# Optimization experiments

Hardware: AMD Instinct MI355X
Metric: run time of the kernel (lower is better)

The kernel has to match this reference:

```python
import jax, jax.numpy as jnp
import numpy as np

FEATURE_DIM = 512
HIDDEN_DIM = 512
N_HEADS = 8
HEAD_DIM = HIDDEN_DIM // N_HEADS
MAX_LEN = 5000
GAMMA = 0.5  # gaussian relative-position bias width
LN_EPS = 1e-5


def make_pe(d_model, max_len):
    # sinusoidal positional encoding buffer, as in PositionalEncoding.__init__
    pos = jnp.arange(max_len, dtype=jnp.float32)[:, None]
    div = jnp.exp(jnp.arange(0, d_model, 2, dtype=jnp.float32) * (-np.log(10000.0) / d_model))
    ang = pos * div  # [max_len, d_model/2]
    pe = jnp.zeros((max_len, d_model), dtype=jnp.float32)
    pe = pe.at[:, 0::2].set(jnp.sin(ang)).at[:, 1::2].set(jnp.cos(ang))
    return pe


def setup_inputs() -> dict:
    key = jax.random.key(0)
    k_x, k_q, k_k, k_v = jax.random.split(key, 4)
    xavier = np.sqrt(6.0 / (FEATURE_DIM + HEAD_DIM))  # xavier_uniform over last two dims
    return {
        "data_window": jax.random.normal(k_x, (1, 2048, FEATURE_DIM), dtype=jnp.float32),
        "W_query": jax.random.uniform(k_q, (N_HEADS, FEATURE_DIM, HEAD_DIM), jnp.float32, -xavier, xavier),
        "W_key": jax.random.uniform(k_k, (N_HEADS, FEATURE_DIM, HEAD_DIM), jnp.float32, -xavier, xavier),
        "W_value": jax.random.uniform(k_v, (N_HEADS, FEATURE_DIM, HEAD_DIM), jnp.float32, -xavier, xavier),
        "ln_gamma": jnp.ones((FEATURE_DIM,), dtype=jnp.float32),
        "ln_beta": jnp.zeros((FEATURE_DIM,), dtype=jnp.float32),
    }


def reference(data_window, W_query, W_key, W_value, ln_gamma, ln_beta):
    B, S, F = data_window.shape
    temperature = 1.0

    # LayerNorm over feature dim
    mu = jnp.mean(data_window, axis=-1, keepdims=True)
    var = jnp.mean(jnp.square(data_window - mu), axis=-1, keepdims=True)
    x = (data_window - mu) * jax.lax.rsqrt(var + LN_EPS) * ln_gamma + ln_beta

    # positional encoding, exactly as original: x + pe[:x.shape[0]] (requires B==1)
    pe = make_pe(FEATURE_DIM, MAX_LEN)
    x = x + pe[:B]  # [B,F] broadcasts over [B,S,F] only because B==1

    # per-head QKV projections, vectorized over heads
    Q = jnp.einsum('bsf,hfd->bhsd', x, W_query)
    K = jnp.einsum('bsf,hfd->bhsd', x, W_key)
    V = jnp.einsum('bsf,hfd->bhsd', x, W_value)

    scores = jnp.einsum('bhsd,bhtd->bhst', Q, K) / np.sqrt(HEAD_DIM)

    # gaussian relative-position bias: scale(=1) * exp(-gamma * (i-j)^2)
    p = jnp.arange(S, dtype=jnp.float32)
    rel = p[:, None] - p[None, :]
    bias = jnp.exp(-GAMMA * jnp.square(rel))  # [S,S]
    scores = (scores + bias[None, None]) / temperature
    # dropout on scores is identity in eval mode

    attn = jax.nn.softmax(scores, axis=-1)  # [B,H,S,S]
    head_out = jnp.einsum('bhst,bhtd->bhsd', attn, V)

    # concat heads along feature dim: [B,S,H*D]
    multi_head_output = head_out.transpose(0, 2, 1, 3).reshape(B, S, N_HEADS * HEAD_DIM)
    mean_weights = jnp.mean(attn, axis=1)  # [B,S,S]
    return multi_head_output, mean_weights
```

## Files before the change

### kernel.cpp

```cpp
#include <hip/hip_runtime.h>
#include <hip/hip_bf16.h>
#include <math.h>

#define S_LEN 2048
#define FDIM  512
#define NH    8
#define HD    64
#define MH_ELEMS (S_LEN * FDIM)
#define MEAN_ELEMS (S_LEN * S_LEN)

typedef _Float16 half_t;
typedef _Float16 half2v __attribute__((ext_vector_type(2)));
typedef _Float16 half4v __attribute__((ext_vector_type(4)));
typedef _Float16 half8v __attribute__((ext_vector_type(8)));
typedef float    float4v __attribute__((ext_vector_type(4)));
typedef int      int4v   __attribute__((ext_vector_type(4)));
typedef unsigned short ushort4v __attribute__((ext_vector_type(4)));

#define MFMA16(a, b, c) __builtin_amdgcn_mfma_f32_16x16x32_f16((a), (b), (c), 0, 0, 0)

static __device__ __forceinline__ unsigned short f2bf(float x) {
    union { __hip_bfloat16 b; unsigned short u; } cv;
    cv.b = __float2bfloat16(x);
    return cv.u;
}

__global__ __launch_bounds__(256) void ln_pe_kernel(const float* __restrict__ x,
                                                    const float* __restrict__ gamma,
                                                    const float* __restrict__ beta,
                                                    half_t* __restrict__ xo) {
    const int row = blockIdx.x;
    const int tid = threadIdx.x;
    const float2 v = ((const float2*)(x + (size_t)row * FDIM))[tid];
    float s = v.x + v.y;
    float q = v.x * v.x + v.y * v.y;
    #pragma unroll
    for (int off = 1; off < 64; off <<= 1) {
        s += __shfl_xor(s, off, 64);
        q += __shfl_xor(q, off, 64);
    }
    __shared__ float red[8];
    const int wave = tid >> 6;
    if ((tid & 63) == 0) { red[wave] = s; red[4 + wave] = q; }
    __syncthreads();
    s = red[0] + red[1] + red[2] + red[3];
    q = red[4] + red[5] + red[6] + red[7];
    const float mu  = s * (1.0f / FDIM);
    const float var = q * (1.0f / FDIM) - mu * mu;
    const float rstd = rsqrtf(var + 1e-5f);
    const int f0 = tid * 2, f1 = tid * 2 + 1;
    const float o0 = (v.x - mu) * rstd * gamma[f0] + beta[f0];
    const float o1 = (v.y - mu) * rstd * gamma[f1] + beta[f1] + 1.0f;
    half2v o; o.x = (half_t)o0; o.y = (half_t)o1;
    ((half2v*)(xo + (size_t)row * FDIM))[tid] = o;
}

__global__ __launch_bounds__(256) void wt_kernel(const float* __restrict__ Wq,
                                                 const float* __restrict__ Wk,
                                                 const float* __restrict__ Wv,
                                                 half_t* __restrict__ WT) {
    const int k0 = blockIdx.x * 64;
    const int h  = blockIdx.y, z = blockIdx.z;
    const float* W = ((z == 0) ? Wq : (z == 1) ? Wk : Wv) + (size_t)h * FDIM * HD;
    __shared__ float Ls[64][65];
    const int tid = threadIdx.x;
    {
        const int kk = tid >> 2, dg = (tid & 3) * 16;
        #pragma unroll
        for (int j = 0; j < 4; ++j) {
            const float4 w = *(const float4*)(W + (size_t)(k0 + kk) * HD + dg + j * 4);
            Ls[kk][dg + j * 4 + 0] = w.x; Ls[kk][dg + j * 4 + 1] = w.y;
            Ls[kk][dg + j * 4 + 2] = w.z; Ls[kk][dg + j * 4 + 3] = w.w;
        }
    }
    __syncthreads();
    {
        const int d = tid >> 2, kg = (tid & 3) * 16;
        half8v t0, t1;
        #pragma unroll
        for (int j = 0; j < 8; ++j) t0[j] = (half_t)Ls[kg + j][d];
        #pragma unroll
        for (int j = 0; j < 8; ++j) t1[j] = (half_t)Ls[kg + 8 + j][d];
        half_t* dst = WT + ((size_t)(z * NH + h) * HD + d) * FDIM + k0 + kg;
        *(half8v*)dst = t0;
        *(half8v*)(dst + 8) = t1;
    }
}

__global__ __launch_bounds__(256) void qkv_kernel(const half_t* __restrict__ xh,
                                                  const half_t* __restrict__ WT,
                                                  half_t* __restrict__ Qo,
                                                  half_t* __restrict__ Ko,
                                                  half_t* __restrict__ VTo) {
    const int ms0 = blockIdx.x * 64;
    const int h   = blockIdx.y, z = blockIdx.z;
    const half_t* Wt = WT + (size_t)(z * NH + h) * HD * FDIM;

    const int tid = threadIdx.x;
    const int wv = tid >> 6, lane = tid & 63;
    const int lo = lane & 15, qq = lane >> 4;

    float4v acc[4];
    #pragma unroll
    for (int cg = 0; cg < 4; ++cg) acc[cg] = (float4v){0.f, 0.f, 0.f, 0.f};

    const half_t* arow = xh + (size_t)(ms0 + wv * 16 + lo) * FDIM + qq * 8;
    const half_t* wrow[4];
    #pragma unroll
    for (int cg = 0; cg < 4; ++cg) wrow[cg] = Wt + (size_t)(cg * 16 + lo) * FDIM + qq * 8;

    half8v a0 = *(const half8v*)(arow), a1 = *(const half8v*)(arow + 32);
    half8v b0[4], b1[4];
    #pragma unroll
    for (int cg = 0; cg < 4; ++cg) { b0[cg] = *(const half8v*)(wrow[cg]); b1[cg] = *(const half8v*)(wrow[cg] + 32); }

    for (int k0 = 0; k0 < FDIM; k0 += 64) {
        const int kn0 = (k0 + 64 < FDIM) ? k0 + 64 : 0;
        const int kn1 = (k0 + 96 < FDIM) ? k0 + 96 : 0;
        half8v an0 = *(const half8v*)(arow + kn0);
        half8v bn0[4];
        #pragma unroll
        for (int cg = 0; cg < 4; ++cg) bn0[cg] = *(const half8v*)(wrow[cg] + kn0);
        #pragma unroll
        for (int cg = 0; cg < 4; ++cg) acc[cg] = MFMA16(a0, b0[cg], acc[cg]);
        half8v an1 = *(const half8v*)(arow + kn1);
        half8v bn1[4];
        #pragma unroll
        for (int cg = 0; cg < 4; ++cg) bn1[cg] = *(const half8v*)(wrow[cg] + kn1);
        #pragma unroll
        for (int cg = 0; cg < 4; ++cg) acc[cg] = MFMA16(a1, b1[cg], acc[cg]);
        a0 = an0; a1 = an1;
        #pragma unroll
        for (int cg = 0; cg < 4; ++cg) { b0[cg] = bn0[cg]; b1[cg] = bn1[cg]; }
    }

    __shared__ float Ls[64][65];
    if (z < 2) {
        half_t* Co = ((z == 0) ? Qo : Ko) + (size_t)h * S_LEN * HD;
        #pragma unroll
        for (int cg = 0; cg < 4; ++cg)
            #pragma unroll
            for (int r = 0; r < 4; ++r)
                Co[(size_t)(ms0 + wv * 16 + qq * 4 + r) * HD + cg * 16 + lo] = (half_t)acc[cg][r];
    } else {
        #pragma unroll
        for (int cg = 0; cg < 4; ++cg)
            #pragma unroll
            for (int r = 0; r < 4; ++r)
                Ls[wv * 16 + qq * 4 + r][cg * 16 + lo] = acc[cg][r];
        __syncthreads();
        const int d = tid & 63, sg = tid >> 6;
        half8v t0, t1;
        #pragma unroll
        for (int j = 0; j < 8; ++j) t0[j] = (half_t)Ls[sg * 16 + j][d];
        #pragma unroll
        for (int j = 0; j < 8; ++j) t1[j] = (half_t)Ls[sg * 16 + 8 + j][d];
        half_t* dst = VTo + (size_t)(h * HD + d) * S_LEN + ms0 + sg * 16;
        *(half8v*)dst = t0;
        *(half8v*)(dst + 8) = t1;
    }
}

__global__ __launch_bounds__(256) void attn2_kernel(const half_t* __restrict__ Qw,
                                                    const half_t* __restrict__ Kw,
                                                    const half_t* __restrict__ VT,
                                                    unsigned short* __restrict__ Praw,
                                                    half_t* __restrict__ Op,
                                                    float* __restrict__ mp,
                                                    float* __restrict__ lp) {
    const int s0 = blockIdx.x * 16;
    const int h  = blockIdx.y;
    const int z  = blockIdx.z;
    const half_t* Qh = Qw + (size_t)h * S_LEN * HD;
    const half_t* Kh = Kw + (size_t)h * S_LEN * HD;
    const half_t* Vt = VT + (size_t)h * (size_t)HD * S_LEN;

    __shared__ float Osh[4][16][65];
    __shared__ float lsh[4][16];
    __shared__ float msh[4][16];

    const int tid = threadIdx.x;
    const int wv = tid >> 6, lane = tid & 63;
    const int lo = lane & 15, qq = lane >> 4;
    const int tb = z * 1024 + wv * 256;

    const half8v q0 = *(const half8v*)(Qh + (size_t)(s0 + lo) * HD + qq * 8);
    const half8v q1 = *(const half8v*)(Qh + (size_t)(s0 + lo) * HD + 32 + qq * 8);

    float4v accO[4];
    #pragma unroll
    for (int dt = 0; dt < 4; ++dt) accO[dt] = (float4v){0.f, 0.f, 0.f, 0.f};
    float m = 0.f;
    float lsum = 0.f;

    const int srcLow  = lo + ((qq & 1) * 2) * 16;
    const int srcHigh = srcLow + 16;
    const bool sel1 = (qq >> 1) != 0;

    unsigned short* prb = Praw + ((size_t)h << 22) + (size_t)(s0 + lo) * S_LEN + qq * 4;

    half8v kc[4], vc[4];
    {
        const half_t* kp0 = Kh + (size_t)(tb + lo) * HD;
        const half_t* kp1 = Kh + (size_t)(tb + 16 + lo) * HD;
        kc[0] = *(const half8v*)(kp0 + qq * 8);
        kc[1] = *(const half8v*)(kp0 + 32 + qq * 8);
        kc[2] = *(const half8v*)(kp1 + qq * 8);
        kc[3] = *(const half8v*)(kp1 + 32 + qq * 8);
        #pragma unroll
        for (int dt = 0; dt < 4; ++dt)
            vc[dt] = *(const half8v*)(Vt + (size_t)(dt * 16 + lo) * S_LEN + tb + qq * 8);
    }

    for (int ps = 0; ps < 8; ++ps) {
        const int Tg  = tb + ps * 32;
        const int Tgn = tb + ((ps < 7) ? ps + 1 : ps) * 32;
        half8v kn[4], vn[4];
        {
            const half_t* kp0 = Kh + (size_t)(Tgn + lo) * HD;
            const half_t* kp1 = Kh + (size_t)(Tgn + 16 + lo) * HD;
            kn[0] = *(const half8v*)(kp0 + qq * 8);
            kn[1] = *(const half8v*)(kp0 + 32 + qq * 8);
            kn[2] = *(const half8v*)(kp1 + qq * 8);
            kn[3] = *(const half8v*)(kp1 + 32 + qq * 8);
            #pragma unroll
            for (int dt = 0; dt < 4; ++dt)
                vn[dt] = *(const half8v*)(Vt + (size_t)(dt * 16 + lo) * S_LEN + Tgn + qq * 8);
        }
        float4v c0 = (float4v){0.f, 0.f, 0.f, 0.f};
        c0 = MFMA16(kc[0], q0, c0);
        c0 = MFMA16(kc[1], q1, c0);
        float4v c1 = (float4v){0.f, 0.f, 0.f, 0.f};
        c1 = MFMA16(kc[2], q0, c1);
        c1 = MFMA16(kc[3], q1, c1);

        float S0[4], S1[4];
        const int dd0 = s0 - Tg;
        const bool near0 = (dd0 > -40) && (dd0 < 40);
        const bool near1 = (dd0 - 16 > -40) && (dd0 - 16 < 40);
        #pragma unroll
        for (int r = 0; r < 4; ++r) {
            float s = c0[r] * 0.125f;
            if (near0) {
                const float d = (float)(s0 + lo - (Tg + qq * 4 + r));
                s += __expf(-0.5f * d * d);
            }
            S0[r] = s;
            float t = c1[r] * 0.125f;
            if (near1) {
                const float d = (float)(s0 + lo - (Tg + 16 + qq * 4 + r));
                t += __expf(-0.5f * d * d);
            }
            S1[r] = t;
        }
        float smax = fmaxf(fmaxf(fmaxf(S0[0], S0[1]), fmaxf(S0[2], S0[3])),
                           fmaxf(fmaxf(S1[0], S1[1]), fmaxf(S1[2], S1[3])));
        smax = fmaxf(smax, __shfl_xor(smax, 16, 64));
        smax = fmaxf(smax, __shfl_xor(smax, 32, 64));
        const float mn = fmaxf(m, smax);
        const float alpha = __expf(m - mn);
        m = mn;
        float E0[4], E1[4];
        float ls = 0.f;
        #pragma unroll
        for (int r = 0; r < 4; ++r) {
            E0[r] = __expf(S0[r] - mn);
            E1[r] = __expf(S1[r] - mn);
            ls += E0[r] + E1[r];
        }
        lsum = lsum * alpha + ls;
        #pragma unroll
        for (int dt = 0; dt < 4; ++dt)
            #pragma unroll
            for (int i = 0; i < 4; ++i) accO[dt][i] *= alpha;

        {
            const float emn = __expf(mn);
            ushort4v ep0, ep1;
            #pragma unroll
            for (int r = 0; r < 4; ++r) {
                ep0[r] = f2bf(E0[r] * emn);
                ep1[r] = f2bf(E1[r] * emn);
            }
            unsigned short* pr = prb + Tg;
            *(ushort4v*)pr = ep0;
            *(ushort4v*)(pr + 16) = ep1;
        }

        int pk0, pk1, pk2, pk3;
        {
            half2v p;
            p.x = (half_t)E0[0]; p.y = (half_t)E0[1];
            pk0 = __builtin_bit_cast(int, p);
            p.x = (half_t)E0[2]; p.y = (half_t)E0[3];
            pk1 = __builtin_bit_cast(int, p);
            p.x = (half_t)E1[0]; p.y = (half_t)E1[1];
            pk2 = __builtin_bit_cast(int, p);
            p.x = (half_t)E1[2]; p.y = (half_t)E1[3];
            pk3 = __builtin_bit_cast(int, p);
        }
        int4v bi;
        {
            const int l0a = __shfl(pk0, srcLow, 64),  l0b = __shfl(pk2, srcLow, 64);
            const int l1a = __shfl(pk1, srcLow, 64),  l1b = __shfl(pk3, srcLow, 64);
            const int h0a = __shfl(pk0, srcHigh, 64), h0b = __shfl(pk2, srcHigh, 64);
            const int h1a = __shfl(pk1, srcHigh, 64), h1b = __shfl(pk3, srcHigh, 64);
            bi[0] = sel1 ? l0b : l0a;
            bi[1] = sel1 ? l1b : l1a;
            bi[2] = sel1 ? h0b : h0a;
            bi[3] = sel1 ? h1b : h1a;
        }
        const half8v bp = __builtin_bit_cast(half8v, bi);
        #pragma unroll
        for (int dt = 0; dt < 4; ++dt) accO[dt] = MFMA16(vc[dt], bp, accO[dt]);

        #pragma unroll
        for (int i = 0; i < 4; ++i) { kc[i] = kn[i]; vc[i] = vn[i]; }
    }

    lsum += __shfl_xor(lsum, 16, 64);
    lsum += __shfl_xor(lsum, 32, 64);
    if (qq == 0) { lsh[wv][lo] = lsum; msh[wv][lo] = m; }
    #pragma unroll
    for (int dt = 0; dt < 4; ++dt)
        #pragma unroll
        for (int r = 0; r < 4; ++r)
            Osh[wv][lo][dt * 16 + qq * 4 + r] = accO[dt][r];
    __syncthreads();

    {
        const int q = tid >> 4, dg = tid & 15;
        const float m0 = msh[0][q], m1 = msh[1][q], m2 = msh[2][q], m3 = msh[3][q];
        const float M = fmaxf(fmaxf(m0, m1), fmaxf(m2, m3));
        const float f0 = __expf(m0 - M), f1 = __expf(m1 - M);
        const float f2 = __expf(m2 - M), f3 = __expf(m3 - M);
        const float L = lsh[0][q] * f0 + lsh[1][q] * f1 + lsh[2][q] * f2 + lsh[3][q] * f3;
        half4v o;
        #pragma unroll
        for (int i = 0; i < 4; ++i) {
            const float ov = Osh[0][q][dg * 4 + i] * f0 + Osh[1][q][dg * 4 + i] * f1 +
                             Osh[2][q][dg * 4 + i] * f2 + Osh[3][q][dg * 4 + i] * f3;
            o[i] = (half_t)ov;
        }
        const size_t pidx = (size_t)(z * NH + h) * S_LEN + s0 + q;
        *(half4v*)(Op + pidx * HD + dg * 4) = o;
        if (dg == 0) { mp[pidx] = M; lp[pidx] = L; }
    }
}

__global__ __launch_bounds__(256) void merge_kernel(const half_t* __restrict__ Op,
                                                    const float* __restrict__ mp,
                                                    const float* __restrict__ lp,
                                                    float* __restrict__ linv,
                                                    float* __restrict__ out) {
    const int s0 = blockIdx.x * 16, h = blockIdx.y;
    const int tid = threadIdx.x, q = tid >> 4, dg = tid & 15;
    const size_t i0 = (size_t)h * S_LEN + s0 + q;
    const size_t i1 = (size_t)(NH + h) * S_LEN + s0 + q;
    const float m0 = mp[i0], m1 = mp[i1], l0 = lp[i0], l1 = lp[i1];
    const float M = fmaxf(m0, m1);
    const float f0 = __expf(m0 - M), f1 = __expf(m1 - M);
    const float L = l0 * f0 + l1 * f1;
    const float inv = 1.0f / L;
    const half4v o0 = *(const half4v*)(Op + i0 * HD + dg * 4);
    const half4v o1 = *(const half4v*)(Op + i1 * HD + dg * 4);
    float4 o;
    o.x = ((float)o0[0] * f0 + (float)o1[0] * f1) * inv;
    o.y = ((float)o0[1] * f0 + (float)o1[1] * f1) * inv;
    o.z = ((float)o0[2] * f0 + (float)o1[2] * f1) * inv;
    o.w = ((float)o0[3] * f0 + (float)o1[3] * f1) * inv;
    *(float4*)(out + (size_t)(s0 + q) * FDIM + h * HD + dg * 4) = o;
    if (dg == 0) linv[(size_t)h * S_LEN + s0 + q] = __expf(-M) * inv;
}

__global__ __launch_bounds__(256) void mean_kernel(const unsigned short* __restrict__ Praw,
                                                   const float* __restrict__ linv,
                                                   float* __restrict__ out) {
    const size_t idx = ((size_t)blockIdx.x * 256 + threadIdx.x) * 8;
    const int q = (int)(idx >> 11);
    float acc[8] = {0.f, 0.f, 0.f, 0.f, 0.f, 0.f, 0.f, 0.f};
    #pragma unroll
    for (int h = 0; h < NH; ++h) {
        const uint4 u = *(const uint4*)(Praw + ((size_t)h << 22) + idx);
        const float li = linv[h * S_LEN + q];
        const unsigned int uu[4] = {u.x, u.y, u.z, u.w};
        #pragma unroll
        for (int j = 0; j < 4; ++j) {
            const float a = __builtin_bit_cast(float, uu[j] << 16);
            const float b = __builtin_bit_cast(float, uu[j] & 0xFFFF0000u);
            acc[2 * j]     += a * li;
            acc[2 * j + 1] += b * li;
        }
    }
    float* o = out + MH_ELEMS + idx;
    *(float4*)o       = make_float4(acc[0] * 0.125f, acc[1] * 0.125f, acc[2] * 0.125f, acc[3] * 0.125f);
    *(float4*)(o + 4) = make_float4(acc[4] * 0.125f, acc[5] * 0.125f, acc[6] * 0.125f, acc[7] * 0.125f);
}

extern "C" void kernel_launch(void* const* d_in, const int* in_sizes, int n_in,
                              void* d_out, int out_size, void* d_ws, size_t ws_size,
                              hipStream_t stream) {
    const float* x  = (const float*)d_in[0];
    const float* Wq = (const float*)d_in[1];
    const float* Wk = (const float*)d_in[2];
    const float* Wv = (const float*)d_in[3];
    const float* g  = (const float*)d_in[4];
    const float* b  = (const float*)d_in[5];
    float* out = (float*)d_out;
    char*  ws  = (char*)d_ws;

    half_t* Qh   = (half_t*)(ws);
    half_t* Kh   = (half_t*)(ws + (2ull  << 20));
    half_t* VT   = (half_t*)(ws + (4ull  << 20));
    half_t* xh   = (half_t*)(ws + (6ull  << 20));
    half_t* WT   = (half_t*)(ws + (8ull  << 20));
    half_t* Op   = (half_t*)(ws + (10ull << 20));
    float*  mp   = (float*) (ws + (14ull << 20));
    float*  lp   = (float*) (ws + (14ull << 20) + (128ull << 10));
    float*  linv = (float*) (ws + (14ull << 20) + (512ull << 10));
    unsigned short* Praw = (unsigned short*)(ws + (16ull << 20));

    ln_pe_kernel<<<S_LEN, 256, 0, stream>>>(x, g, b, xh);
    wt_kernel<<<dim3(8, 8, 3), 256, 0, stream>>>(Wq, Wk, Wv, WT);
    qkv_kernel<<<dim3(32, 8, 3), 256, 0, stream>>>(xh, WT, Qh, Kh, VT);
    attn2_kernel<<<dim3(128, 8, 2), 256, 0, stream>>>(Qh, Kh, VT, Praw, Op, mp, lp);
    merge_kernel<<<dim3(128, 8), 256, 0, stream>>>(Op, mp, lp, linv, out);
    mean_kernel<<<MEAN_ELEMS / 8 / 256, 256, 0, stream>>>(Praw, linv, out);
}
```

Measured before the change: 185.1 us.

## Fuse prep and merge kernels, double per-block rows in QKV and attention

```diff
diff --git a/kernel.cpp b/kernel.cpp
--- a/kernel.cpp
+++ b/kernel.cpp
@@ -25,65 +25,67 @@
     return cv.u;
 }
 
-__global__ __launch_bounds__(256) void ln_pe_kernel(const float* __restrict__ x,
-                                                    const float* __restrict__ gamma,
-                                                    const float* __restrict__ beta,
-                                                    half_t* __restrict__ xo) {
-    const int row = blockIdx.x;
+__global__ __launch_bounds__(256) void prep_kernel(const float* __restrict__ x,
+                                                   const float* __restrict__ gamma,
+                                                   const float* __restrict__ beta,
+                                                   const float* __restrict__ Wq,
+                                                   const float* __restrict__ Wk,
+                                                   const float* __restrict__ Wv,
+                                                   half_t* __restrict__ xo,
+                                                   half_t* __restrict__ WT) {
     const int tid = threadIdx.x;
-    const float2 v = ((const float2*)(x + (size_t)row * FDIM))[tid];
-    float s = v.x + v.y;
-    float q = v.x * v.x + v.y * v.y;
-    #pragma unroll
-    for (int off = 1; off < 64; off <<= 1) {
-        s += __shfl_xor(s, off, 64);
-        q += __shfl_xor(q, off, 64);
-    }
-    __shared__ float red[8];
-    const int wave = tid >> 6;
-    if ((tid & 63) == 0) { red[wave] = s; red[4 + wave] = q; }
-    __syncthreads();
-    s = red[0] + red[1] + red[2] + red[3];
-    q = red[4] + red[5] + red[6] + red[7];
-    const float mu  = s * (1.0f / FDIM);
-    const float var = q * (1.0f / FDIM) - mu * mu;
-    const float rstd = rsqrtf(var + 1e-5f);
-    const int f0 = tid * 2, f1 = tid * 2 + 1;
-    const float o0 = (v.x - mu) * rstd * gamma[f0] + beta[f0];
-    const float o1 = (v.y - mu) * rstd * gamma[f1] + beta[f1] + 1.0f;
-    half2v o; o.x = (half_t)o0; o.y = (half_t)o1;
-    ((half2v*)(xo + (size_t)row * FDIM))[tid] = o;
-}
-
-__global__ __launch_bounds__(256) void wt_kernel(const float* __restrict__ Wq,
-                                                 const float* __restrict__ Wk,
-                                                 const float* __restrict__ Wv,
-                                                 half_t* __restrict__ WT) {
-    const int k0 = blockIdx.x * 64;
-    const int h  = blockIdx.y, z = blockIdx.z;
-    const float* W = ((z == 0) ? Wq : (z == 1) ? Wk : Wv) + (size_t)h * FDIM * HD;
-    __shared__ float Ls[64][65];
-    const int tid = threadIdx.x;
-    {
-        const int kk = tid >> 2, dg = (tid & 3) * 16;
-        #pragma unroll
-        for (int j = 0; j < 4; ++j) {
-            const float4 w = *(const float4*)(W + (size_t)(k0 + kk) * HD + dg + j * 4);
-            Ls[kk][dg + j * 4 + 0] = w.x; Ls[kk][dg + j * 4 + 1] = w.y;
-            Ls[kk][dg + j * 4 + 2] = w.z; Ls[kk][dg + j * 4 + 3] = w.w;
-        }
-    }
-    __syncthreads();
-    {
-        const int d = tid >> 2, kg = (tid & 3) * 16;
-        half8v t0, t1;
-        #pragma unroll
-        for (int j = 0; j < 8; ++j) t0[j] = (half_t)Ls[kg + j][d];
-        #pragma unroll
-        for (int j = 0; j < 8; ++j) t1[j] = (half_t)Ls[kg + 8 + j][d];
-        half_t* dst = WT + ((size_t)(z * NH + h) * HD + d) * FDIM + k0 + kg;
-        *(half8v*)dst = t0;
-        *(half8v*)(dst + 8) = t1;
+    if (blockIdx.x < 2048) {
+        const int row = blockIdx.x;
+        const float2 v = ((const float2*)(x + (size_t)row * FDIM))[tid];
+        float s = v.x + v.y;
+        float q = v.x * v.x + v.y * v.y;
+        #pragma unroll
+        for (int off = 1; off < 64; off <<= 1) {
+            s += __shfl_xor(s, off, 64);
+            q += __shfl_xor(q, off, 64);
+        }
+        __shared__ float red[8];
+        const int wave = tid >> 6;
+        if ((tid & 63) == 0) { red[wave] = s; red[4 + wave] = q; }
+        __syncthreads();
+        s = red[0] + red[1] + red[2] + red[3];
+        q = red[4] + red[5] + red[6] + red[7];
+        const float mu  = s * (1.0f / FDIM);
+        const float var = q * (1.0f / FDIM) - mu * mu;
+        const float rstd = rsqrtf(var + 1e-5f);
+        const int f0 = tid * 2, f1 = tid * 2 + 1;
+        const float o0 = (v.x - mu) * rstd * gamma[f0] + beta[f0];
+        const float o1 = (v.y - mu) * rstd * gamma[f1] + beta[f1] + 1.0f;
+        half2v o; o.x = (half_t)o0; o.y = (half_t)o1;
+        ((half2v*)(xo + (size_t)row * FDIM))[tid] = o;
+    } else {
+        const int idx = blockIdx.x - 2048;
+        const int k0 = (idx & 7) * 64;
+        const int h  = (idx >> 3) & 7;
+        const int z  = idx >> 6;
+        const float* W = ((z == 0) ? Wq : (z == 1) ? Wk : Wv) + (size_t)h * FDIM * HD;
+        __shared__ float Ls[64][65];
+        {
+            const int kk = tid >> 2, dg = (tid & 3) * 16;
+            #pragma unroll
+            for (int j = 0; j < 4; ++j) {
+                const float4 w = *(const float4*)(W + (size_t)(k0 + kk) * HD + dg + j * 4);
+                Ls[kk][dg + j * 4 + 0] = w.x; Ls[kk][dg + j * 4 + 1] = w.y;
+                Ls[kk][dg + j * 4 + 2] = w.z; Ls[kk][dg + j * 4 + 3] = w.w;
+            }
+        }
+        __syncthreads();
+        {
+            const int d = tid >> 2, kg = (tid & 3) * 16;
+            half8v t0, t1;
+            #pragma unroll
+            for (int j = 0; j < 8; ++j) t0[j] = (half_t)Ls[kg + j][d];
+            #pragma unroll
+            for (int j = 0; j < 8; ++j) t1[j] = (half_t)Ls[kg + 8 + j][d];
+            half_t* dst = WT + ((size_t)(z * NH + h) * HD + d) * FDIM + k0 + kg;
+            *(half8v*)dst = t0;
+            *(half8v*)(dst + 8) = t1;
+        }
     }
 }
 
@@ -92,7 +94,7 @@
                                                   half_t* __restrict__ Qo,
                                                   half_t* __restrict__ Ko,
                                                   half_t* __restrict__ VTo) {
-    const int ms0 = blockIdx.x * 64;
+    const int ms0 = blockIdx.x * 128;
     const int h   = blockIdx.y, z = blockIdx.z;
     const half_t* Wt = WT + (size_t)(z * NH + h) * HD * FDIM;
 
@@ -100,64 +102,75 @@
     const int wv = tid >> 6, lane = tid & 63;
     const int lo = lane & 15, qq = lane >> 4;
 
-    float4v acc[4];
-    #pragma unroll
-    for (int cg = 0; cg < 4; ++cg) acc[cg] = (float4v){0.f, 0.f, 0.f, 0.f};
-
-    const half_t* arow = xh + (size_t)(ms0 + wv * 16 + lo) * FDIM + qq * 8;
+    float4v acc[2][4];
+    #pragma unroll
+    for (int rg = 0; rg < 2; ++rg)
+        #pragma unroll
+        for (int cg = 0; cg < 4; ++cg) acc[rg][cg] = (float4v){0.f, 0.f, 0.f, 0.f};
+
+    const half_t* ar[2];
+    ar[0] = xh + (size_t)(ms0 + wv * 32 + lo) * FDIM + qq * 8;
+    ar[1] = ar[0] + 16 * FDIM;
     const half_t* wrow[4];
     #pragma unroll
     for (int cg = 0; cg < 4; ++cg) wrow[cg] = Wt + (size_t)(cg * 16 + lo) * FDIM + qq * 8;
 
-    half8v a0 = *(const half8v*)(arow), a1 = *(const half8v*)(arow + 32);
-    half8v b0[4], b1[4];
-    #pragma unroll
-    for (int cg = 0; cg < 4; ++cg) { b0[cg] = *(const half8v*)(wrow[cg]); b1[cg] = *(const half8v*)(wrow[cg] + 32); }
+    half8v a_c[2][2], b_c[4][2];
+    #pragma unroll
+    for (int rg = 0; rg < 2; ++rg) { a_c[rg][0] = *(const half8v*)(ar[rg]); a_c[rg][1] = *(const half8v*)(ar[rg] + 32); }
+    #pragma unroll
+    for (int cg = 0; cg < 4; ++cg) { b_c[cg][0] = *(const half8v*)(wrow[cg]); b_c[cg][1] = *(const half8v*)(wrow[cg] + 32); }
 
     for (int k0 = 0; k0 < FDIM; k0 += 64) {
         const int kn0 = (k0 + 64 < FDIM) ? k0 + 64 : 0;
         const int kn1 = (k0 + 96 < FDIM) ? k0 + 96 : 0;
-        half8v an0 = *(const half8v*)(arow + kn0);
-        half8v bn0[4];
-        #pragma unroll
-        for (int cg = 0; cg < 4; ++cg) bn0[cg] = *(const half8v*)(wrow[cg] + kn0);
-        #pragma unroll
-        for (int cg = 0; cg < 4; ++cg) acc[cg] = MFMA16(a0, b0[cg], acc[cg]);
-        half8v an1 = *(const half8v*)(arow + kn1);
-        half8v bn1[4];
-        #pragma unroll
-        for (int cg = 0; cg < 4; ++cg) bn1[cg] = *(const half8v*)(wrow[cg] + kn1);
-        #pragma unroll
-        for (int cg = 0; cg < 4; ++cg) acc[cg] = MFMA16(a1, b1[cg], acc[cg]);
-        a0 = an0; a1 = an1;
-        #pragma unroll
-        for (int cg = 0; cg < 4; ++cg) { b0[cg] = bn0[cg]; b1[cg] = bn1[cg]; }
-    }
-
-    __shared__ float Ls[64][65];
+        half8v a_n[2][2], b_n[4][2];
+        #pragma unroll
+        for (int rg = 0; rg < 2; ++rg) { a_n[rg][0] = *(const half8v*)(ar[rg] + kn0); a_n[rg][1] = *(const half8v*)(ar[rg] + kn1); }
+        #pragma unroll
+        for (int cg = 0; cg < 4; ++cg) { b_n[cg][0] = *(const half8v*)(wrow[cg] + kn0); b_n[cg][1] = *(const half8v*)(wrow[cg] + kn1); }
+        #pragma unroll
+        for (int kh = 0; kh < 2; ++kh)
+            #pragma unroll
+            for (int rg = 0; rg < 2; ++rg)
+                #pragma unroll
+                for (int cg = 0; cg < 4; ++cg)
+                    acc[rg][cg] = MFMA16(a_c[rg][kh], b_c[cg][kh], acc[rg][cg]);
+        #pragma unroll
+        for (int rg = 0; rg < 2; ++rg) { a_c[rg][0] = a_n[rg][0]; a_c[rg][1] = a_n[rg][1]; }
+        #pragma unroll
+        for (int cg = 0; cg < 4; ++cg) { b_c[cg][0] = b_n[cg][0]; b_c[cg][1] = b_n[cg][1]; }
+    }
+
     if (z < 2) {
         half_t* Co = ((z == 0) ? Qo : Ko) + (size_t)h * S_LEN * HD;
         #pragma unroll
-        for (int cg = 0; cg < 4; ++cg)
-            #pragma unroll
-            for (int r = 0; r < 4; ++r)
-                Co[(size_t)(ms0 + wv * 16 + qq * 4 + r) * HD + cg * 16 + lo] = (half_t)acc[cg][r];
+        for (int rg = 0; rg < 2; ++rg)
+            #pragma unroll
+            for (int cg = 0; cg < 4; ++cg)
+                #pragma unroll
+                for (int r = 0; r < 4; ++r)
+                    Co[(size_t)(ms0 + wv * 32 + rg * 16 + qq * 4 + r) * HD + cg * 16 + lo] =
+                        (half_t)acc[rg][cg][r];
     } else {
-        #pragma unroll
-        for (int cg = 0; cg < 4; ++cg)
-            #pragma unroll
-            for (int r = 0; r < 4; ++r)
-                Ls[wv * 16 + qq * 4 + r][cg * 16 + lo] = acc[cg][r];
+        __shared__ float Ls[128][65];
+        #pragma unroll
+        for (int rg = 0; rg < 2; ++rg)
+            #pragma unroll
+            for (int cg = 0; cg < 4; ++cg)
+                #pragma unroll
+                for (int r = 0; r < 4; ++r)
+                    Ls[wv * 32 + rg * 16 + qq * 4 + r][cg * 16 + lo] = acc[rg][cg][r];
         __syncthreads();
         const int d = tid & 63, sg = tid >> 6;
-        half8v t0, t1;
-        #pragma unroll
-        for (int j = 0; j < 8; ++j) t0[j] = (half_t)Ls[sg * 16 + j][d];
-        #pragma unroll
-        for (int j = 0; j < 8; ++j) t1[j] = (half_t)Ls[sg * 16 + 8 + j][d];
-        half_t* dst = VTo + (size_t)(h * HD + d) * S_LEN + ms0 + sg * 16;
-        *(half8v*)dst = t0;
-        *(half8v*)(dst + 8) = t1;
+        half_t* dst = VTo + (size_t)(h * HD + d) * S_LEN + ms0 + sg * 32;
+        #pragma unroll
+        for (int c = 0; c < 4; ++c) {
+            half8v t;
+            #pragma unroll
+            for (int j = 0; j < 8; ++j) t[j] = (half_t)Ls[sg * 32 + c * 8 + j][d];
+            *(half8v*)(dst + c * 8) = t;
+        }
     }
 }
 
@@ -168,38 +181,43 @@
                                                     half_t* __restrict__ Op,
                                                     float* __restrict__ mp,
                                                     float* __restrict__ lp) {
-    const int s0 = blockIdx.x * 16;
+    const int s0 = blockIdx.x * 32;
     const int h  = blockIdx.y;
     const int z  = blockIdx.z;
     const half_t* Qh = Qw + (size_t)h * S_LEN * HD;
     const half_t* Kh = Kw + (size_t)h * S_LEN * HD;
     const half_t* Vt = VT + (size_t)h * (size_t)HD * S_LEN;
 
-    __shared__ float Osh[4][16][65];
-    __shared__ float lsh[4][16];
-    __shared__ float msh[4][16];
+    __shared__ float Osh[4][32][65];
+    __shared__ float lsh[4][32];
+    __shared__ float msh[4][32];
 
     const int tid = threadIdx.x;
     const int wv = tid >> 6, lane = tid & 63;
     const int lo = lane & 15, qq = lane >> 4;
     const int tb = z * 1024 + wv * 256;
 
-    const half8v q0 = *(const half8v*)(Qh + (size_t)(s0 + lo) * HD + qq * 8);
-    const half8v q1 = *(const half8v*)(Qh + (size_t)(s0 + lo) * HD + 32 + qq * 8);
-
-    float4v accO[4];
-    #pragma unroll
-    for (int dt = 0; dt < 4; ++dt) accO[dt] = (float4v){0.f, 0.f, 0.f, 0.f};
-    float m = 0.f;
-    float lsum = 0.f;
+    const half8v qA0 = *(const half8v*)(Qh + (size_t)(s0 + lo) * HD + qq * 8);
+    const half8v qA1 = *(const half8v*)(Qh + (size_t)(s0 + lo) * HD + 32 + qq * 8);
+    const half8v qB0 = *(const half8v*)(Qh + (size_t)(s0 + 16 + lo) * HD + qq * 8);
+    const half8v qB1 = *(const half8v*)(Qh + (size_t)(s0 + 16 + lo) * HD + 32 + qq * 8);
+
+    float4v accA[4], accB[4];
+    #pragma unroll
+    for (int dt = 0; dt < 4; ++dt) {
+        accA[dt] = (float4v){0.f, 0.f, 0.f, 0.f};
+        accB[dt] = (float4v){0.f, 0.f, 0.f, 0.f};
+    }
+    float mA = 0.f, mB = 0.f, lA = 0.f, lB = 0.f;
 
     const int srcLow  = lo + ((qq & 1) * 2) * 16;
     const int srcHigh = srcLow + 16;
     const bool sel1 = (qq >> 1) != 0;
 
-    unsigned short* prb = Praw + ((size_t)h << 22) + (size_t)(s0 + lo) * S_LEN + qq * 4;
-
-    half8v kc[4], vc[4];
+    unsigned short* prA = Praw + ((size_t)h << 22) + (size_t)(s0 + lo) * S_LEN + qq * 4;
+    unsigned short* prB = prA + 16 * S_LEN;
+
+    half8v kc[4];
     {
         const half_t* kp0 = Kh + (size_t)(tb + lo) * HD;
         const half_t* kp1 = Kh + (size_t)(tb + 16 + lo) * HD;
@@ -207,15 +225,12 @@
         kc[1] = *(const half8v*)(kp0 + 32 + qq * 8);
         kc[2] = *(const half8v*)(kp1 + qq * 8);
         kc[3] = *(const half8v*)(kp1 + 32 + qq * 8);
-        #pragma unroll
-        for (int dt = 0; dt < 4; ++dt)
-            vc[dt] = *(const half8v*)(Vt + (size_t)(dt * 16 + lo) * S_LEN + tb + qq * 8);
     }
 
     for (int ps = 0; ps < 8; ++ps) {
         const int Tg  = tb + ps * 32;
         const int Tgn = tb + ((ps < 7) ? ps + 1 : ps) * 32;
-        half8v kn[4], vn[4];
+        half8v kn[4], vc[4];
         {
             const half_t* kp0 = Kh + (size_t)(Tgn + lo) * HD;
             const half_t* kp1 = Kh + (size_t)(Tgn + 16 + lo) * HD;
@@ -225,111 +240,139 @@
             kn[3] = *(const half8v*)(kp1 + 32 + qq * 8);
             #pragma unroll
             for (int dt = 0; dt < 4; ++dt)
-                vn[dt] = *(const half8v*)(Vt + (size_t)(dt * 16 + lo) * S_LEN + Tgn + qq * 8);
-        }
-        float4v c0 = (float4v){0.f, 0.f, 0.f, 0.f};
-        c0 = MFMA16(kc[0], q0, c0);
-        c0 = MFMA16(kc[1], q1, c0);
-        float4v c1 = (float4v){0.f, 0.f, 0.f, 0.f};
-        c1 = MFMA16(kc[2], q0, c1);
-        c1 = MFMA16(kc[3], q1, c1);
-
-        float S0[4], S1[4];
+                vc[dt] = *(const half8v*)(Vt + (size_t)(dt * 16 + lo) * S_LEN + Tg + qq * 8);
+        }
+        float4v c0A = (float4v){0.f, 0.f, 0.f, 0.f};
+        c0A = MFMA16(kc[0], qA0, c0A); c0A = MFMA16(kc[1], qA1, c0A);
+        float4v c1A = (float4v){0.f, 0.f, 0.f, 0.f};
+        c1A = MFMA16(kc[2], qA0, c1A); c1A = MFMA16(kc[3], qA1, c1A);
+        float4v c0B = (float4v){0.f, 0.f, 0.f, 0.f};
+        c0B = MFMA16(kc[0], qB0, c0B); c0B = MFMA16(kc[1], qB1, c0B);
+        float4v c1B = (float4v){0.f, 0.f, 0.f, 0.f};
+        c1B = MFMA16(kc[2], qB0, c1B); c1B = MFMA16(kc[3], qB1, c1B);
+
         const int dd0 = s0 - Tg;
-        const bool near0 = (dd0 > -40) && (dd0 < 40);
-        const bool near1 = (dd0 - 16 > -40) && (dd0 - 16 < 40);
+        const bool nA0 = (dd0 > -40) && (dd0 < 40);
+        const bool nA1 = (dd0 - 16 > -40) && (dd0 - 16 < 40);
+        const bool nB0 = (dd0 + 16 > -40) && (dd0 + 16 < 40);
+        const bool nB1 = nA0;
+        float S0A[4], S1A[4], S0B[4], S1B[4];
         #pragma unroll
         for (int r = 0; r < 4; ++r) {
-            float s = c0[r] * 0.125f;
-            if (near0) {
-                const float d = (float)(s0 + lo - (Tg + qq * 4 + r));
-                s += __expf(-0.5f * d * d);
+            const int t0 = Tg + qq * 4 + r, t1 = t0 + 16;
+            float sa0 = c0A[r] * 0.125f;
+            if (nA0) { const float d = (float)(s0 + lo - t0); sa0 += __expf(-0.5f * d * d); }
+            float sa1 = c1A[r] * 0.125f;
+            if (nA1) { const float d = (float)(s0 + lo - t1); sa1 += __expf(-0.5f * d * d); }
+            float sb0 = c0B[r] * 0.125f;
+            if (nB0) { const float d = (float)(s0 + 16 + lo - t0); sb0 += __expf(-0.5f * d * d); }
+            float sb1 = c1B[r] * 0.125f;
+            if (nB1) { const float d = (float)(s0 + 16 + lo - t1); sb1 += __expf(-0.5f * d * d); }
+            S0A[r] = sa0; S1A[r] = sa1; S0B[r] = sb0; S1B[r] = sb1;
+        }
+        float smA = fmaxf(fmaxf(fmaxf(S0A[0], S0A[1]), fmaxf(S0A[2], S0A[3])),
+                          fmaxf(fmaxf(S1A[0], S1A[1]), fmaxf(S1A[2], S1A[3])));
+        float smB = fmaxf(fmaxf(fmaxf(S0B[0], S0B[1]), fmaxf(S0B[2], S0B[3])),
+                          fmaxf(fmaxf(S1B[0], S1B[1]), fmaxf(S1B[2], S1B[3])));
+        smA = fmaxf(smA, __shfl_xor(smA, 16, 64));
+        smA = fmaxf(smA, __shfl_xor(smA, 32, 64));
+        smB = fmaxf(smB, __shfl_xor(smB, 16, 64));
+        smB = fmaxf(smB, __shfl_xor(smB, 32, 64));
+        const float mnA = fmaxf(mA, smA), mnB = fmaxf(mB, smB);
+        const float alA = __expf(mA - mnA), alB = __expf(mB - mnB);
+        mA = mnA; mB = mnB;
+        float E0A[4], E1A[4], E0B[4], E1B[4];
+        float lsA = 0.f, lsB = 0.f;
+        #pragma unroll
+        for (int r = 0; r < 4; ++r) {
+            E0A[r] = __expf(S0A[r] - mnA); E1A[r] = __expf(S1A[r] - mnA);
+            E0B[r] = __expf(S0B[r] - mnB); E1B[r] = __expf(S1B[r] - mnB);
+            lsA += E0A[r] + E1A[r];
+            lsB += E0B[r] + E1B[r];
+        }
+        lA = lA * alA + lsA;
+        lB = lB * alB + lsB;
+        #pragma unroll
+        for (int dt = 0; dt < 4; ++dt)
+            #pragma unroll
+            for (int i = 0; i < 4; ++i) { accA[dt][i] *= alA; accB[dt][i] *= alB; }
+
+        {
+            const float emA = __expf(mnA), emB = __expf(mnB);
+            ushort4v e0a, e1a, e0b, e1b;
+            #pragma unroll
+            for (int r = 0; r < 4; ++r) {
+                e0a[r] = f2bf(E0A[r] * emA); e1a[r] = f2bf(E1A[r] * emA);
+                e0b[r] = f2bf(E0B[r] * emB); e1b[r] = f2bf(E1B[r] * emB);
             }
-            S0[r] = s;
-            float t = c1[r] * 0.125f;
-            if (near1) {
-                const float d = (float)(s0 + lo - (Tg + 16 + qq * 4 + r));
-                t += __expf(-0.5f * d * d);
-            }
-            S1[r] = t;
-        }
-        float smax = fmaxf(fmaxf(fmaxf(S0[0], S0[1]), fmaxf(S0[2], S0[3])),
-                           fmaxf(fmaxf(S1[0], S1[1]), fmaxf(S1[2], S1[3])));
-        smax = fmaxf(smax, __shfl_xor(smax, 16, 64));
-        smax = fmaxf(smax, __shfl_xor(smax, 32, 64));
-        const float mn = fmaxf(m, smax);
-        const float alpha = __expf(m - mn);
-        m = mn;
-        float E0[4], E1[4];
-        float ls = 0.f;
+            *(ushort4v*)(prA + Tg)      = e0a;
+            *(ushort4v*)(prA + Tg + 16) = e1a;
+            *(ushort4v*)(prB + Tg)      = e0b;
+            *(ushort4v*)(prB + Tg + 16) = e1b;
+        }
+
+        int pkA0, pkA1, pkA2, pkA3, pkB0, pkB1, pkB2, pkB3;
+        {
+            half2v p;
+            p.x = (half_t)E0A[0]; p.y = (half_t)E0A[1]; pkA0 = __builtin_bit_cast(int, p);
+            p.x = (half_t)E0A[2]; p.y = (half_t)E0A[3]; pkA1 = __builtin_bit_cast(int, p);
+            p.x = (half_t)E1A[0]; p.y = (half_t)E1A[1]; pkA2 = __builtin_bit_cast(int, p);
+            p.x = (half_t)E1A[2]; p.y = (half_t)E1A[3]; pkA3 = __builtin_bit_cast(int, p);
+            p.x = (half_t)E0B[0]; p.y = (half_t)E0B[1]; pkB0 = __builtin_bit_cast(int, p);
+            p.x = (half_t)E0B[2]; p.y = (half_t)E0B[3]; pkB1 = __builtin_bit_cast(int, p);
+            p.x = (half_t)E1B[0]; p.y = (half_t)E1B[1]; pkB2 = __builtin_bit_cast(int, p);
+            p.x = (half_t)E1B[2]; p.y = (half_t)E1B[3]; pkB3 = __builtin_bit_cast(int, p);
+        }
+        int4v biA, biB;
+        {
+            const int l0a = __shfl(pkA0, srcLow, 64),  l0b = __shfl(pkA2, srcLow, 64);
+            const int l1a = __shfl(pkA1, srcLow, 64),  l1b = __shfl(pkA3, srcLow, 64);
+            const int h0a = __shfl(pkA0, srcHigh, 64), h0b = __shfl(pkA2, srcHigh, 64);
+            const int h1a = __shfl(pkA1, srcHigh, 64), h1b = __shfl(pkA3, srcHigh, 64);
+            biA[0] = sel1 ? l0b : l0a;
+            biA[1] = sel1 ? l1b : l1a;
+            biA[2] = sel1 ? h0b : h0a;
+            biA[3] = sel1 ? h1b : h1a;
+        }
+        {
+            const int l0a = __shfl(pkB0, srcLow, 64),  l0b = __shfl(pkB2, srcLow, 64);
+            const int l1a = __shfl(pkB1, srcLow, 64),  l1b = __shfl(pkB3, srcLow, 64);
+            const int h0a = __shfl(pkB0, srcHigh, 64), h0b = __shfl(pkB2, srcHigh, 64);
+            const int h1a = __shfl(pkB1, srcHigh, 64), h1b = __shfl(pkB3, srcHigh, 64);
+            biB[0] = sel1 ? l0b : l0a;
+            biB[1] = sel1 ? l1b : l1a;
+            biB[2] = sel1 ? h0b : h0a;
+            biB[3] = sel1 ? h1b : h1a;
+        }
+        const half8v bpA = __builtin_bit_cast(half8v, biA);
+        const half8v bpB = __builtin_bit_cast(half8v, biB);
+        #pragma unroll
+        for (int dt = 0; dt < 4; ++dt) {
+            accA[dt] = MFMA16(vc[dt], bpA, accA[dt]);
+            accB[dt] = MFMA16(vc[dt], bpB, accB[dt]);
+        }
+        #pragma unroll
+        for (int i = 0; i < 4; ++i) kc[i] = kn[i];
+    }
+
+    lA += __shfl_xor(lA, 16, 64); lA += __shfl_xor(lA, 32, 64);
+    lB += __shfl_xor(lB, 16, 64); lB += __shfl_xor(lB, 32, 64);
+    if (qq == 0) {
+        lsh[wv][lo] = lA;      msh[wv][lo] = mA;
+        lsh[wv][16 + lo] = lB; msh[wv][16 + lo] = mB;
+    }
+    #pragma unroll
+    for (int dt = 0; dt < 4; ++dt)
         #pragma unroll
         for (int r = 0; r < 4; ++r) {
-            E0[r] = __expf(S0[r] - mn);
-            E1[r] = __expf(S1[r] - mn);
-            ls += E0[r] + E1[r];
-        }
-        lsum = lsum * alpha + ls;
-        #pragma unroll
-        for (int dt = 0; dt < 4; ++dt)
-            #pragma unroll
-            for (int i = 0; i < 4; ++i) accO[dt][i] *= alpha;
-
-        {
-            const float emn = __expf(mn);
-            ushort4v ep0, ep1;
-            #pragma unroll
-            for (int r = 0; r < 4; ++r) {
-                ep0[r] = f2bf(E0[r] * emn);
-                ep1[r] = f2bf(E1[r] * emn);
-            }
-            unsigned short* pr = prb + Tg;
-            *(ushort4v*)pr = ep0;
-            *(ushort4v*)(pr + 16) = ep1;
-        }
-
-        int pk0, pk1, pk2, pk3;
-        {
-            half2v p;
-            p.x = (half_t)E0[0]; p.y = (half_t)E0[1];
-            pk0 = __builtin_bit_cast(int, p);
-            p.x = (half_t)E0[2]; p.y = (half_t)E0[3];
-            pk1 = __builtin_bit_cast(int, p);
-            p.x = (half_t)E1[0]; p.y = (half_t)E1[1];
-            pk2 = __builtin_bit_cast(int, p);
-            p.x = (half_t)E1[2]; p.y = (half_t)E1[3];
-            pk3 = __builtin_bit_cast(int, p);
-        }
-        int4v bi;
-        {
-            const int l0a = __shfl(pk0, srcLow, 64),  l0b = __shfl(pk2, srcLow, 64);
-            const int l1a = __shfl(pk1, srcLow, 64),  l1b = __shfl(pk3, srcLow, 64);
-            const int h0a = __shfl(pk0, srcHigh, 64), h0b = __shfl(pk2, srcHigh, 64);
-            const int h1a = __shfl(pk1, srcHigh, 64), h1b = __shfl(pk3, srcHigh, 64);
-            bi[0] = sel1 ? l0b : l0a;
-            bi[1] = sel1 ? l1b : l1a;
-            bi[2] = sel1 ? h0b : h0a;
-            bi[3] = sel1 ? h1b : h1a;
-        }
-        const half8v bp = __builtin_bit_cast(half8v, bi);
-        #pragma unroll
-        for (int dt = 0; dt < 4; ++dt) accO[dt] = MFMA16(vc[dt], bp, accO[dt]);
-
-        #pragma unroll
-        for (int i = 0; i < 4; ++i) { kc[i] = kn[i]; vc[i] = vn[i]; }
-    }
-
-    lsum += __shfl_xor(lsum, 16, 64);
-    lsum += __shfl_xor(lsum, 32, 64);
-    if (qq == 0) { lsh[wv][lo] = lsum; msh[wv][lo] = m; }
-    #pragma unroll
-    for (int dt = 0; dt < 4; ++dt)
-        #pragma unroll
-        for (int r = 0; r < 4; ++r)
-            Osh[wv][lo][dt * 16 + qq * 4 + r] = accO[dt][r];
+            Osh[wv][lo][dt * 16 + qq * 4 + r]      = accA[dt][r];
+            Osh[wv][16 + lo][dt * 16 + qq * 4 + r] = accB[dt][r];
+        }
     __syncthreads();
 
-    {
-        const int q = tid >> 4, dg = tid & 15;
+    #pragma unroll
+    for (int p = 0; p < 2; ++p) {
+        const int q = p * 16 + (tid >> 4), dg = tid & 15;
         const float m0 = msh[0][q], m1 = msh[1][q], m2 = msh[2][q], m3 = msh[3][q];
         const float M = fmaxf(fmaxf(m0, m1), fmaxf(m2, m3));
         const float f0 = __expf(m0 - M), f1 = __expf(m1 - M);
@@ -348,53 +391,53 @@
     }
 }
 
-__global__ __launch_bounds__(256) void merge_kernel(const half_t* __restrict__ Op,
-                                                    const float* __restrict__ mp,
-                                                    const float* __restrict__ lp,
-                                                    float* __restrict__ linv,
-                                                    float* __restrict__ out) {
-    const int s0 = blockIdx.x * 16, h = blockIdx.y;
-    const int tid = threadIdx.x, q = tid >> 4, dg = tid & 15;
-    const size_t i0 = (size_t)h * S_LEN + s0 + q;
-    const size_t i1 = (size_t)(NH + h) * S_LEN + s0 + q;
-    const float m0 = mp[i0], m1 = mp[i1], l0 = lp[i0], l1 = lp[i1];
-    const float M = fmaxf(m0, m1);
-    const float f0 = __expf(m0 - M), f1 = __expf(m1 - M);
-    const float L = l0 * f0 + l1 * f1;
-    const float inv = 1.0f / L;
-    const half4v o0 = *(const half4v*)(Op + i0 * HD + dg * 4);
-    const half4v o1 = *(const half4v*)(Op + i1 * HD + dg * 4);
-    float4 o;
-    o.x = ((float)o0[0] * f0 + (float)o1[0] * f1) * inv;
-    o.y = ((float)o0[1] * f0 + (float)o1[1] * f1) * inv;
-    o.z = ((float)o0[2] * f0 + (float)o1[2] * f1) * inv;
-    o.w = ((float)o0[3] * f0 + (float)o1[3] * f1) * inv;
-    *(float4*)(out + (size_t)(s0 + q) * FDIM + h * HD + dg * 4) = o;
-    if (dg == 0) linv[(size_t)h * S_LEN + s0 + q] = __expf(-M) * inv;
-}
-
-__global__ __launch_bounds__(256) void mean_kernel(const unsigned short* __restrict__ Praw,
-                                                   const float* __restrict__ linv,
-                                                   float* __restrict__ out) {
-    const size_t idx = ((size_t)blockIdx.x * 256 + threadIdx.x) * 8;
-    const int q = (int)(idx >> 11);
-    float acc[8] = {0.f, 0.f, 0.f, 0.f, 0.f, 0.f, 0.f, 0.f};
-    #pragma unroll
-    for (int h = 0; h < NH; ++h) {
-        const uint4 u = *(const uint4*)(Praw + ((size_t)h << 22) + idx);
-        const float li = linv[h * S_LEN + q];
-        const unsigned int uu[4] = {u.x, u.y, u.z, u.w};
-        #pragma unroll
-        for (int j = 0; j < 4; ++j) {
-            const float a = __builtin_bit_cast(float, uu[j] << 16);
-            const float b = __builtin_bit_cast(float, uu[j] & 0xFFFF0000u);
-            acc[2 * j]     += a * li;
-            acc[2 * j + 1] += b * li;
-        }
-    }
-    float* o = out + MH_ELEMS + idx;
-    *(float4*)o       = make_float4(acc[0] * 0.125f, acc[1] * 0.125f, acc[2] * 0.125f, acc[3] * 0.125f);
-    *(float4*)(o + 4) = make_float4(acc[4] * 0.125f, acc[5] * 0.125f, acc[6] * 0.125f, acc[7] * 0.125f);
+__global__ __launch_bounds__(256) void meanmerge_kernel(const half_t* __restrict__ Op,
+                                                        const float* __restrict__ mp,
+                                                        const float* __restrict__ lp,
+                                                        const unsigned short* __restrict__ Praw,
+                                                        float* __restrict__ out) {
+    const int q = blockIdx.x;
+    const int tid = threadIdx.x;
+    __shared__ float lish[NH];
+    {
+        const int h = tid >> 5, t32 = tid & 31;
+        const size_t i0 = (size_t)h * S_LEN + q;
+        const size_t i1 = (size_t)(NH + h) * S_LEN + q;
+        const float m0 = mp[i0], m1 = mp[i1];
+        const float M = fmaxf(m0, m1);
+        const float f0 = __expf(m0 - M), f1 = __expf(m1 - M);
+        const float L = lp[i0] * f0 + lp[i1] * f1;
+        const float inv = 1.0f / L;
+        if (t32 == 0) lish[h] = __expf(-M) * inv;
+        const int d = t32 * 2;
+        const half2v o0 = *(const half2v*)(Op + i0 * HD + d);
+        const half2v o1 = *(const half2v*)(Op + i1 * HD + d);
+        float2 o;
+        o.x = ((float)o0.x * f0 + (float)o1.x * f1) * inv;
+        o.y = ((float)o0.y * f0 + (float)o1.y * f1) * inv;
+        *(float2*)(out + (size_t)q * FDIM + h * HD + d) = o;
+    }
+    __syncthreads();
+    {
+        const int idx = tid * 8;
+        float acc[8] = {0.f, 0.f, 0.f, 0.f, 0.f, 0.f, 0.f, 0.f};
+        #pragma unroll
+        for (int h = 0; h < NH; ++h) {
+            const uint4 u = *(const uint4*)(Praw + ((size_t)h << 22) + (size_t)q * S_LEN + idx);
+            const float li = lish[h];
+            const unsigned int uu[4] = {u.x, u.y, u.z, u.w};
+            #pragma unroll
+            for (int j = 0; j < 4; ++j) {
+                const float a = __builtin_bit_cast(float, uu[j] << 16);
+                const float b = __builtin_bit_cast(float, uu[j] & 0xFFFF0000u);
+                acc[2 * j]     += a * li;
+                acc[2 * j + 1] += b * li;
+            }
+        }
+        float* o = out + MH_ELEMS + (size_t)q * S_LEN + idx;
+        *(float4*)o       = make_float4(acc[0] * 0.125f, acc[1] * 0.125f, acc[2] * 0.125f, acc[3] * 0.125f);
+        *(float4*)(o + 4) = make_float4(acc[4] * 0.125f, acc[5] * 0.125f, acc[6] * 0.125f, acc[7] * 0.125f);
+    }
 }
 
 extern "C" void kernel_launch(void* const* d_in, const int* in_sizes, int n_in,
@@ -417,13 +460,10 @@
     half_t* Op   = (half_t*)(ws + (10ull << 20));
     float*  mp   = (float*) (ws + (14ull << 20));
     float*  lp   = (float*) (ws + (14ull << 20) + (128ull << 10));
-    float*  linv = (float*) (ws + (14ull << 20) + (512ull << 10));
     unsigned short* Praw = (unsigned short*)(ws + (16ull << 20));
 
-    ln_pe_kernel<<<S_LEN, 256, 0, stream>>>(x, g, b, xh);
-    wt_kernel<<<dim3(8, 8, 3), 256, 0, stream>>>(Wq, Wk, Wv, WT);
-    qkv_kernel<<<dim3(32, 8, 3), 256, 0, stream>>>(xh, WT, Qh, Kh, VT);
-    attn2_kernel<<<dim3(128, 8, 2), 256, 0, stream>>>(Qh, Kh, VT, Praw, Op, mp, lp);
-    merge_kernel<<<dim3(128, 8), 256, 0, stream>>>(Op, mp, lp, linv, out);
-    mean_kernel<<<MEAN_ELEMS / 8 / 256, 256, 0, stream>>>(Praw, linv, out);
-}
+    prep_kernel<<<2240, 256, 0, stream>>>(x, g, b, Wq, Wk, Wv, xh, WT);
+    qkv_kernel<<<dim3(16, 8, 3), 256, 0, stream>>>(xh, WT, Qh, Kh, VT);
+    attn2_kernel<<<dim3(64, 8, 2), 256, 0, stream>>>(Qh, Kh, VT, Praw, Op, mp, lp);
+    meanmerge_kernel<<<S_LEN, 256, 0, stream>>>(Op, mp, lp, Praw, out);
+}
```

Measured after the change: 158.4 us. 14.4% less time.
